# Kernel optimization log

Hardware: AMD Instinct MI355X
Metric: run time of the kernel (lower is better)

## Reference

```python
import jax, jax.numpy as jnp
import numpy as np

PAD = 7                 # init padding
T = 2 * PAD + 1         # T_side_dense = 15 shifts per axis
LAMDA = 1.0             # init lamda
EPS = 1e-16             # hardcoded epsilon in the torch loss body


def _joint_hist(x_out, x_tf_out):
    # Equivalent of F.conv2d(x_out.permute(1,0,2,3), weight=x_tf_out.permute(1,0,2,3), padding=PAD)
    # expressed as T*T shifted matmuls (correlation / cost-volume form).
    bn, k, h, w = x_out.shape
    A = jnp.transpose(x_out, (1, 0, 2, 3))      # (k, bn, h, w)  conv "input"
    B = jnp.transpose(x_tf_out, (1, 0, 2, 3))   # (k, bn, h, w)  conv "weight"
    A_pad = jnp.pad(A, ((0, 0), (0, 0), (PAD, PAD), (PAD, PAD)))

    def step(carry, s):
        dy, dx = s // T, s % T
        sl = jax.lax.dynamic_slice(A_pad, (0, 0, dy, dx), (k, bn, h, w))
        # p[n, o] at this shift = sum_{c,y,x} A_pad[n,c,y+dy,x+dx] * B[o,c,y,x]
        return carry, jnp.einsum('nchw,ochw->no', sl, B)

    _, p = jax.lax.scan(step, None, jnp.arange(T * T))
    # (T*T, k, k) -> (T, T, k, k); matches torch p_i_j.permute(2, 3, 0, 1)
    return p.reshape(T, T, k, k)


def reference(x_out, x_tf_out):
    p = _joint_hist(x_out, x_tf_out)
    # shift to positive; min is detached in torch -> stop_gradient
    p = p - jax.lax.stop_gradient(p.min()) + EPS
    # normalize per shift over the (k, k) joint
    p = p / p.sum(axis=(2, 3), keepdims=True)
    # symmetrize
    p = (p + jnp.swapaxes(p, 2, 3)) / 2.0
    p_i = p.sum(axis=2, keepdims=True)   # (T, T, 1, k) marginal (broadcasts like repeat)
    p_j = p.sum(axis=3, keepdims=True)   # (T, T, k, 1) marginal
    loss = (-p * (jnp.log(p + EPS)
                  - LAMDA * jnp.log(p_i + EPS)
                  - LAMDA * jnp.log(p_j + EPS))).sum() / (T * T)
    return loss


def setup_inputs() -> dict:
    key = jax.random.key(0)
    k1, k2 = jax.random.split(key)
    bn, k, h, w = 16, 10, 224, 224
    # simplex over axis=1 is asserted by the torch module -> use softmax
    x_out = jax.nn.softmax(jax.random.normal(k1, (bn, k, h, w), dtype=jnp.float32), axis=1)
    x_tf_out = jax.nn.softmax(jax.random.normal(k2, (bn, k, h, w), dtype=jnp.float32), axis=1)
    return {"x_out": x_out, "x_tf_out": x_tf_out}
```

## Files before the change

### kernel.cpp

```cpp
#include <hip/hip_runtime.h>
#include <stdint.h>
#include <math.h>


#define PADV 7
#define TS 15
#define KCLS 10
#define HH 224
#define WW 224
#define MD 160
#define NCELL (MD*MD)
#define NBLK 256
#define TY 14
#define BSTRIDE 232
#define BPH 240
#define PLANEE 2408
#define ABUFE (8*PLANEE)
#define LEPS 1e-16

typedef __attribute__((ext_vector_type(4))) float f32x4;
typedef __attribute__((ext_vector_type(8))) short bf16x8;

__device__ __forceinline__ unsigned short f2bf(float f) {
  union { float f; uint32_t u; } v; v.f = f;
  return (unsigned short)((v.u + 0x7FFFu + ((v.u >> 16) & 1u)) >> 16);
}

__device__ __forceinline__ uint32_t pack2bf(float a, float b) {
  return (uint32_t)f2bf(a) | ((uint32_t)f2bf(b) << 16);
}

__device__ __forceinline__ void glds16(const unsigned short* g, unsigned short* l) {
  __builtin_amdgcn_global_load_lds(
      (const __attribute__((address_space(1))) unsigned int*)g,
      (__attribute__((address_space(3))) unsigned int*)l, 16, 0, 0);
}

__device__ __forceinline__ void plane_write(const f32x4 f[4], unsigned short* awr) {
  uint32_t w[8];
#pragma unroll
  for (int k = 0; k < 8; ++k)
    w[k] = pack2bf(f[k >> 1][(k & 1) * 2], f[k >> 1][(k & 1) * 2 + 1]);
#pragma unroll
  for (int c = 0; c < 8; ++c) {
    union { uint32_t u[4]; uint4 v; } o;
    if (c & 1) {
#pragma unroll
      for (int j = 0; j < 4; ++j) o.u[j] = w[j + (c + 1) / 2];
    } else {
#pragma unroll
      for (int j = 0; j < 4; ++j)
        o.u[j] = __builtin_amdgcn_alignbit(w[j + 1 + c / 2], w[j + c / 2], 16);
    }
    *(uint4*)(awr + c * PLANEE) = o.v;
  }
}

__global__ __launch_bounds__(256)
void prep_b(const float* __restrict__ xt, unsigned short* __restrict__ bp) {
  const int idx   = blockIdx.x * 256 + threadIdx.x;
  const int rowid = idx / 29;
  const int chunk = idx - rowid * 29;
  const int x0    = chunk * 8;
  const int yy    = rowid % BPH;
  const int cls   = rowid / BPH;
  const int row   = yy - PADV;
  union { unsigned short h[8]; uint4 v; } out;
  if (row >= 0 && row < HH && x0 < WW) {
    const float* src = xt + ((size_t)cls * HH + row) * WW + x0;
#pragma unroll
    for (int j = 0; j < 8; ++j) out.h[j] = f2bf(src[j]);
  } else {
    out.v = make_uint4(0u, 0u, 0u, 0u);
  }
  *(uint4*)(bp + (size_t)rowid * BSTRIDE + x0) = out.v;
}

__global__ __launch_bounds__(640, 3)
void corr_gemm(const float* __restrict__ xo, const unsigned short* __restrict__ bpad,
               float* __restrict__ partials) {
  __shared__ __align__(16) unsigned short ldsA8[2 * ABUFE];
  __shared__ __align__(16) unsigned short ldsB[KCLS * 16 * BSTRIDE];

  const int tid  = threadIdx.x;
  const int bid0 = blockIdx.x;
  const int bid  = (bid0 & 7) * 32 + (bid0 >> 3);
  const int b    = bid >> 4;
  const int y0   = (bid & 15) * TY;

  const int lane = tid & 63;
  const int wv   = tid >> 6;
  const int wm   = wv >> 1;
  const int wn   = wv & 1;
  const int quad = lane >> 4;
  const int l15  = lane & 15;

  f32x4 acc[2][5];
#pragma unroll
  for (int i = 0; i < 2; ++i)
#pragma unroll
    for (int j = 0; j < 5; ++j) acc[i][j] = (f32x4){0.f, 0.f, 0.f, 0.f};

  const float* Ab = xo + (size_t)b * KCLS * HH * WW;
  const unsigned short* Bb = bpad + (size_t)b * KCLS * BPH * BSTRIDE;

  const bool aw  = tid < 300;
  const int an   = aw ? tid / 30 : 0;
  const int atp  = aw ? tid - (tid / 30) * 30 : 0;
  const int axb  = atp * 8 - 8;
  bool gv[4];
#pragma unroll
  for (int g = 0; g < 4; ++g)
    gv[g] = aw && (axb + 4 * g >= 0) && (axb + 4 * g + 4 <= WW);
  unsigned short* const awr0 = ldsA8 + an * 240 + atp * 8;

  for (int pr = wv; pr < 15 * KCLS; pr += 10) {
    const int r15  = pr / KCLS;
    const int o    = pr - r15 * KCLS;
    const int yy   = y0 + r15;
    const int slot = (y0 - PADV + r15) & 15;
    if (lane < 29)
      glds16(Bb + ((size_t)o * BPH + yy) * BSTRIDE + lane * 8,
             ldsB + (o * 16 + slot) * BSTRIDE);
  }

  f32x4 f[4];
  {
    const float* src = Ab + ((size_t)an * HH + y0) * WW + axb;
#pragma unroll
    for (int g = 0; g < 4; ++g) {
      f[g] = (f32x4){0.f, 0.f, 0.f, 0.f};
      if (gv[g]) f[g] = *(const f32x4*)(src + 4 * g);
    }
  }
  if (aw) plane_write(f, awr0);
  __syncthreads();

  int cur = 0;
  for (int s = 0; s < TY; ++s) {
    const int y = y0 + s;
    const bool more = (s + 1 < TY);

    if (more) {
      const int yy   = y + 8 + PADV;
      const int slot = (y + 8) & 15;
      if (lane < 29)
        glds16(Bb + ((size_t)wv * BPH + yy) * BSTRIDE + lane * 8,
               ldsB + (wv * 16 + slot) * BSTRIDE);
      const float* src = Ab + ((size_t)an * HH + (y + 1)) * WW + axb;
#pragma unroll
      for (int g = 0; g < 4; ++g) {
        f[g] = (f32x4){0.f, 0.f, 0.f, 0.f};
        if (gv[g]) f[g] = *(const f32x4*)(src + 4 * g);
      }
    }

    const unsigned short* paB = ldsA8 + cur * ABUFE + (l15 & 7) * PLANEE + (l15 & 8);
    const int slotB = (y + PADV - l15) & 15;

#pragma unroll 1
    for (int xc = 0; xc < 7; ++xc) {
      const int x0 = xc * 32;
      bf16x8 afrag[2], bfrag[5];
#pragma unroll
      for (int mi = 0; mi < 2; ++mi)
        afrag[mi] = *(const bf16x8*)(paB + (wm * 2 + mi) * 240 + x0 + quad * 8);
#pragma unroll
      for (int ni = 0; ni < 5; ++ni) {
        const int to = wn * 5 + ni;
        bfrag[ni] = *(const bf16x8*)(ldsB + (to * 16 + slotB) * BSTRIDE + x0 + quad * 8);
      }
#pragma unroll
      for (int mi = 0; mi < 2; ++mi)
#pragma unroll
        for (int ni = 0; ni < 5; ++ni)
          acc[mi][ni] = __builtin_amdgcn_mfma_f32_16x16x32_bf16(
              afrag[mi], bfrag[ni], acc[mi][ni], 0, 0, 0);
    }

    if (more) {
      if (aw) plane_write(f, awr0 + (cur ^ 1) * ABUFE);
      __syncthreads();
      cur ^= 1;
    }
  }

  float* outp = partials + (size_t)bid * NCELL;
#pragma unroll
  for (int mi = 0; mi < 2; ++mi)
#pragma unroll
    for (int ni = 0; ni < 5; ++ni) {
      const int mrow = (wm * 2 + mi) * 16 + quad * 4;
      const int ncol = (wn * 5 + ni) * 16 + l15;
#pragma unroll
      for (int r = 0; r < 4; ++r)
        outp[(size_t)(mrow + r) * MD + ncol] = acc[mi][ni][r];
    }
}

__global__ __launch_bounds__(256)
void reduce_stage1(const float* __restrict__ partials, float* __restrict__ stage2) {
  const int c  = (blockIdx.x % 100) * 256 + threadIdx.x;
  const int pg = blockIdx.x / 100;
  const float* base = partials + (size_t)pg * 32 * NCELL + c;
  float s0 = 0.f, s1 = 0.f, s2 = 0.f, s3 = 0.f;
  for (int p = 0; p < 32; p += 4) {
    s0 += base[(size_t)(p + 0) * NCELL];
    s1 += base[(size_t)(p + 1) * NCELL];
    s2 += base[(size_t)(p + 2) * NCELL];
    s3 += base[(size_t)(p + 3) * NCELL];
  }
  stage2[(size_t)pg * NCELL + c] = (s0 + s1) + (s2 + s3);
}

__global__ __launch_bounds__(256)
void reduce_final(const float* __restrict__ stage2, float* __restrict__ Cout,
                  float* __restrict__ mins, float* __restrict__ dout) {
  const int c = blockIdx.x * 256 + threadIdx.x;
  if (blockIdx.x == 0 && threadIdx.x == 0) dout[0] = 0.f;
  double s = 0.0;
#pragma unroll
  for (int pg = 0; pg < 8; ++pg) s += (double)stage2[(size_t)pg * NCELL + c];
  const float sf = (float)s;
  Cout[c] = sf;
  const int m  = c / MD;
  const int nn = c - m * MD;
  const bool valid = ((m & 15) < TS) && ((nn & 15) < TS);
  __shared__ float red[256];
  red[threadIdx.x] = valid ? sf : 3.4e38f;
  __syncthreads();
  for (int st = 128; st > 0; st >>= 1) {
    if (threadIdx.x < st)
      red[threadIdx.x] = fminf(red[threadIdx.x], red[threadIdx.x + st]);
    __syncthreads();
  }
  if (threadIdx.x == 0) mins[blockIdx.x] = red[0];
}

__global__ __launch_bounds__(128)
void loss_kernel(const float* __restrict__ Cmat, const float* __restrict__ mins,
                 float* __restrict__ dout) {
  const int s   = blockIdx.x;
  const int dy  = s / TS;
  const int dx  = s - dy * TS;
  const int tid = threadIdx.x;
  __shared__ float fm[128];
  __shared__ double q[100];
  __shared__ double sym[100];
  __shared__ double pi[10], pj[10];
  __shared__ double red[128];

  fm[tid] = (tid < 100) ? mins[tid] : 3.4e38f;
  __syncthreads();
  for (int st = 64; st > 0; st >>= 1) {
    if (tid < st) fm[tid] = fminf(fm[tid], fm[tid + st]);
    __syncthreads();
  }
  const double minv = (double)fm[0];
  __syncthreads();

  if (tid < 100) {
    const int n = tid / 10, o = tid - (tid / 10) * 10;
    const double v = (double)Cmat[(size_t)(n * 16 + dx) * MD + (o * 16 + dy)];
    q[tid] = v - minv + LEPS;
  }
  __syncthreads();
  red[tid] = (tid < 100) ? q[tid] : 0.0;
  __syncthreads();
  for (int st = 64; st > 0; st >>= 1) {
    if (tid < st) red[tid] += red[tid + st];
    __syncthreads();
  }
  const double Z = red[0];
  __syncthreads();
  if (tid < 100) {
    const int n = tid / 10, o = tid - (tid / 10) * 10;
    sym[tid] = (q[n * 10 + o] + q[o * 10 + n]) * 0.5 / Z;
  }
  __syncthreads();
  if (tid < 10) {
    double a = 0.0, bsum = 0.0;
    for (int n2 = 0; n2 < 10; ++n2) {
      a    += sym[n2 * 10 + tid];
      bsum += sym[tid * 10 + n2];
    }
    pi[tid] = a;
    pj[tid] = bsum;
  }
  __syncthreads();
  double term = 0.0;
  if (tid < 100) {
    const int n = tid / 10, o = tid - (tid / 10) * 10;
    const double sp = sym[tid];
    term = -sp * (log(sp + LEPS) - log(pi[o] + LEPS) - log(pj[n] + LEPS));
  }
  red[tid] = term;
  __syncthreads();
  for (int st = 64; st > 0; st >>= 1) {
    if (tid < st) red[tid] += red[tid + st];
    __syncthreads();
  }
  if (tid == 0) atomicAdd(dout, (float)(red[0] / (double)(TS * TS)));
}

extern "C" void kernel_launch(void* const* d_in, const int* in_sizes, int n_in,
                              void* d_out, int out_size, void* d_ws, size_t ws_size,
                              hipStream_t stream) {
  const float* xo = (const float*)d_in[0];
  const float* xt = (const float*)d_in[1];
  float* ws       = (float*)d_ws;

  float* partials = ws;
  float* stage2   = partials + (size_t)NBLK * NCELL;
  float* Cmat     = stage2 + (size_t)8 * NCELL;
  float* mins     = Cmat + NCELL;
  unsigned short* bpad = (unsigned short*)(mins + 128);
  float* out      = (float*)d_out;

  hipLaunchKernelGGL(prep_b,        dim3(4350), dim3(256), 0, stream, xt, bpad);
  hipLaunchKernelGGL(corr_gemm,     dim3(NBLK), dim3(640), 0, stream, xo, bpad, partials);
  hipLaunchKernelGGL(reduce_stage1, dim3(800),  dim3(256), 0, stream, partials, stage2);
  hipLaunchKernelGGL(reduce_final,  dim3(100),  dim3(256), 0, stream, stage2, Cmat, mins, out);
  hipLaunchKernelGGL(loss_kernel,   dim3(225),  dim3(128), 0, stream, Cmat, mins, out);
}
```

Measured before the change: 150.9 us.

## Split corr_gemm waves by K-range with LDS reduction and fuse reduce stages

The ten waves in each corr_gemm block are split into two K-groups that cover different x-chunk ranges. Each wave now computes a larger M×N tile, and four of the five waves in a group share their B fragments. The two groups' accumulators are summed through LDS before the block writes its partials, and only the second group issues the B-row prefetch. The two-stage partial reduction is merged into one kernel that reads all 256 partials in double precision, and prep_b loads with float4. In exchange, accumulator register use doubles, occupancy drops to 2 blocks per SM, and the fused reduction runs on only 100 blocks.

```diff
diff --git a/kernel.cpp b/kernel.cpp
--- a/kernel.cpp
+++ b/kernel.cpp
@@ -16,6 +16,8 @@
 #define BPH 240
 #define PLANEE 2408
 #define ABUFE (8*PLANEE)
+#define LDSA_BYTES (2*ABUFE*2)
+#define LDSB_BYTES (KCLS*16*BSTRIDE*2)
 #define LEPS 1e-16
 
 typedef __attribute__((ext_vector_type(4))) float f32x4;
@@ -53,6 +55,57 @@
         o.u[j] = __builtin_amdgcn_alignbit(w[j + 1 + c / 2], w[j + c / 2], 16);
     }
     *(uint4*)(awr + c * PLANEE) = o.v;
+  }
+}
+
+template<int XB, int XE>
+__device__ __forceinline__ void compute_xcs(
+    const unsigned short* __restrict__ paB, const unsigned short* __restrict__ lB,
+    int slotB, bool shareB, int Mb0, int Nb0, int q8, f32x4 (&acc)[2][2][5]) {
+#pragma unroll
+  for (int xc = XB; xc < XE; ++xc) {
+    const int qo = xc * 32 + q8;
+    if (shareB) {
+      bf16x8 bfrag[5];
+#pragma unroll
+      for (int ni = 0; ni < 5; ++ni)
+        bfrag[ni] = *(const bf16x8*)(lB + ((Nb0 + ni) * 16 + slotB) * BSTRIDE + qo);
+#pragma unroll
+      for (int sub = 0; sub < 2; ++sub) {
+        bf16x8 afrag[2];
+#pragma unroll
+        for (int mi = 0; mi < 2; ++mi)
+          afrag[mi] = *(const bf16x8*)(paB + (Mb0 + 2 * sub + mi) * 240 + qo);
+        __builtin_amdgcn_s_setprio(1);
+#pragma unroll
+        for (int mi = 0; mi < 2; ++mi)
+#pragma unroll
+          for (int ni = 0; ni < 5; ++ni)
+            acc[sub][mi][ni] = __builtin_amdgcn_mfma_f32_16x16x32_bf16(
+                afrag[mi], bfrag[ni], acc[sub][mi][ni], 0, 0, 0);
+        __builtin_amdgcn_s_setprio(0);
+      }
+    } else {
+      bf16x8 afrag[2];
+#pragma unroll
+      for (int mi = 0; mi < 2; ++mi)
+        afrag[mi] = *(const bf16x8*)(paB + (Mb0 + mi) * 240 + qo);
+#pragma unroll
+      for (int sub = 0; sub < 2; ++sub) {
+        bf16x8 bfrag[5];
+#pragma unroll
+        for (int ni = 0; ni < 5; ++ni)
+          bfrag[ni] = *(const bf16x8*)(lB + ((5 * sub + ni) * 16 + slotB) * BSTRIDE + qo);
+        __builtin_amdgcn_s_setprio(1);
+#pragma unroll
+        for (int mi = 0; mi < 2; ++mi)
+#pragma unroll
+          for (int ni = 0; ni < 5; ++ni)
+            acc[sub][mi][ni] = __builtin_amdgcn_mfma_f32_16x16x32_bf16(
+                afrag[mi], bfrag[ni], acc[sub][mi][ni], 0, 0, 0);
+        __builtin_amdgcn_s_setprio(0);
+      }
+    }
   }
 }
 
@@ -66,21 +119,26 @@
   const int cls   = rowid / BPH;
   const int row   = yy - PADV;
   union { unsigned short h[8]; uint4 v; } out;
-  if (row >= 0 && row < HH && x0 < WW) {
-    const float* src = xt + ((size_t)cls * HH + row) * WW + x0;
-#pragma unroll
-    for (int j = 0; j < 8; ++j) out.h[j] = f2bf(src[j]);
+  if (row >= 0 && row < HH && chunk < 28) {
+    const float4* src = (const float4*)(xt + ((size_t)cls * HH + row) * WW + x0);
+    const float4 f0 = src[0], f1 = src[1];
+    out.h[0] = f2bf(f0.x); out.h[1] = f2bf(f0.y);
+    out.h[2] = f2bf(f0.z); out.h[3] = f2bf(f0.w);
+    out.h[4] = f2bf(f1.x); out.h[5] = f2bf(f1.y);
+    out.h[6] = f2bf(f1.z); out.h[7] = f2bf(f1.w);
   } else {
     out.v = make_uint4(0u, 0u, 0u, 0u);
   }
   *(uint4*)(bp + (size_t)rowid * BSTRIDE + x0) = out.v;
 }
 
-__global__ __launch_bounds__(640, 3)
+__global__ __launch_bounds__(640, 2)
 void corr_gemm(const float* __restrict__ xo, const unsigned short* __restrict__ bpad,
                float* __restrict__ partials) {
-  __shared__ __align__(16) unsigned short ldsA8[2 * ABUFE];
-  __shared__ __align__(16) unsigned short ldsB[KCLS * 16 * BSTRIDE];
+  __shared__ __align__(16) unsigned char smem[LDSA_BYTES + LDSB_BYTES];
+  unsigned short* const ldsA8 = (unsigned short*)smem;
+  unsigned short* const ldsB  = (unsigned short*)(smem + LDSA_BYTES);
+  float* const scratch        = (float*)smem;
 
   const int tid  = threadIdx.x;
   const int bid0 = blockIdx.x;
@@ -90,16 +148,23 @@
 
   const int lane = tid & 63;
   const int wv   = tid >> 6;
-  const int wm   = wv >> 1;
-  const int wn   = wv & 1;
+  const int kg   = (wv >= 5);
+  const int w5   = kg ? wv - 5 : wv;
   const int quad = lane >> 4;
   const int l15  = lane & 15;
-
-  f32x4 acc[2][5];
-#pragma unroll
-  for (int i = 0; i < 2; ++i)
-#pragma unroll
-    for (int j = 0; j < 5; ++j) acc[i][j] = (f32x4){0.f, 0.f, 0.f, 0.f};
+  const int q8   = quad * 8;
+
+  const bool shareB = (w5 < 4);
+  const int Mb0 = shareB ? (w5 >> 1) * 4 : 8;
+  const int Nb0 = shareB ? (w5 & 1) * 5 : 0;
+
+  f32x4 acc[2][2][5];
+#pragma unroll
+  for (int s2 = 0; s2 < 2; ++s2)
+#pragma unroll
+    for (int i = 0; i < 2; ++i)
+#pragma unroll
+      for (int j = 0; j < 5; ++j) acc[s2][i][j] = (f32x4){0.f, 0.f, 0.f, 0.f};
 
   const float* Ab = xo + (size_t)b * KCLS * HH * WW;
   const unsigned short* Bb = bpad + (size_t)b * KCLS * BPH * BSTRIDE;
@@ -142,11 +207,17 @@
     const bool more = (s + 1 < TY);
 
     if (more) {
-      const int yy   = y + 8 + PADV;
-      const int slot = (y + 8) & 15;
-      if (lane < 29)
-        glds16(Bb + ((size_t)wv * BPH + yy) * BSTRIDE + lane * 8,
-               ldsB + (wv * 16 + slot) * BSTRIDE);
+      if (kg == 1) {
+        const int yy   = y + 8 + PADV;
+        const int slot = (y + 8) & 15;
+#pragma unroll
+        for (int j = 0; j < 2; ++j) {
+          const int ro = w5 * 2 + j;
+          if (lane < 29)
+            glds16(Bb + ((size_t)ro * BPH + yy) * BSTRIDE + lane * 8,
+                   ldsB + (ro * 16 + slot) * BSTRIDE);
+        }
+      }
       const float* src = Ab + ((size_t)an * HH + (y + 1)) * WW + axb;
 #pragma unroll
       for (int g = 0; g < 4; ++g) {
@@ -158,25 +229,10 @@
     const unsigned short* paB = ldsA8 + cur * ABUFE + (l15 & 7) * PLANEE + (l15 & 8);
     const int slotB = (y + PADV - l15) & 15;
 
-#pragma unroll 1
-    for (int xc = 0; xc < 7; ++xc) {
-      const int x0 = xc * 32;
-      bf16x8 afrag[2], bfrag[5];
-#pragma unroll
-      for (int mi = 0; mi < 2; ++mi)
-        afrag[mi] = *(const bf16x8*)(paB + (wm * 2 + mi) * 240 + x0 + quad * 8);
-#pragma unroll
-      for (int ni = 0; ni < 5; ++ni) {
-        const int to = wn * 5 + ni;
-        bfrag[ni] = *(const bf16x8*)(ldsB + (to * 16 + slotB) * BSTRIDE + x0 + quad * 8);
-      }
-#pragma unroll
-      for (int mi = 0; mi < 2; ++mi)
-#pragma unroll
-        for (int ni = 0; ni < 5; ++ni)
-          acc[mi][ni] = __builtin_amdgcn_mfma_f32_16x16x32_bf16(
-              afrag[mi], bfrag[ni], acc[mi][ni], 0, 0, 0);
-    }
+    if (kg == 0)
+      compute_xcs<0, 3>(paB, ldsB, slotB, shareB, Mb0, Nb0, q8, acc);
+    else
+      compute_xcs<3, 7>(paB, ldsB, slotB, shareB, Mb0, Nb0, q8, acc);
 
     if (more) {
       if (aw) plane_write(f, awr0 + (cur ^ 1) * ABUFE);
@@ -185,43 +241,57 @@
     }
   }
 
-  float* outp = partials + (size_t)bid * NCELL;
-#pragma unroll
-  for (int mi = 0; mi < 2; ++mi)
-#pragma unroll
-    for (int ni = 0; ni < 5; ++ni) {
-      const int mrow = (wm * 2 + mi) * 16 + quad * 4;
-      const int ncol = (wn * 5 + ni) * 16 + l15;
-#pragma unroll
-      for (int r = 0; r < 4; ++r)
-        outp[(size_t)(mrow + r) * MD + ncol] = acc[mi][ni][r];
-    }
+  __syncthreads();
+  if (kg == 1) {
+    float* dst = scratch + w5 * 5120 + lane * 4;
+#pragma unroll
+    for (int sub = 0; sub < 2; ++sub)
+#pragma unroll
+      for (int mi = 0; mi < 2; ++mi)
+#pragma unroll
+        for (int ni = 0; ni < 5; ++ni) {
+          const int t = (sub * 2 + mi) * 5 + ni;
+          *(f32x4*)(dst + t * 256) = acc[sub][mi][ni];
+        }
+  }
+  __syncthreads();
+  if (kg == 0) {
+    const float* src = scratch + w5 * 5120 + lane * 4;
+    float* outp = partials + (size_t)bid * NCELL;
+#pragma unroll
+    for (int sub = 0; sub < 2; ++sub)
+#pragma unroll
+      for (int mi = 0; mi < 2; ++mi)
+#pragma unroll
+        for (int ni = 0; ni < 5; ++ni) {
+          const int t = (sub * 2 + mi) * 5 + ni;
+          f32x4 o = *(const f32x4*)(src + t * 256);
+          o += acc[sub][mi][ni];
+          const int tm = shareB ? (Mb0 + 2 * sub + mi) : (8 + mi);
+          const int to = shareB ? (Nb0 + ni) : (5 * sub + ni);
+          const int mrow = tm * 16 + quad * 4;
+          const int ncol = to * 16 + l15;
+#pragma unroll
+          for (int r = 0; r < 4; ++r)
+            outp[(size_t)(mrow + r) * MD + ncol] = o[r];
+        }
+  }
 }
 
 __global__ __launch_bounds__(256)
-void reduce_stage1(const float* __restrict__ partials, float* __restrict__ stage2) {
-  const int c  = (blockIdx.x % 100) * 256 + threadIdx.x;
-  const int pg = blockIdx.x / 100;
-  const float* base = partials + (size_t)pg * 32 * NCELL + c;
-  float s0 = 0.f, s1 = 0.f, s2 = 0.f, s3 = 0.f;
-  for (int p = 0; p < 32; p += 4) {
-    s0 += base[(size_t)(p + 0) * NCELL];
-    s1 += base[(size_t)(p + 1) * NCELL];
-    s2 += base[(size_t)(p + 2) * NCELL];
-    s3 += base[(size_t)(p + 3) * NCELL];
-  }
-  stage2[(size_t)pg * NCELL + c] = (s0 + s1) + (s2 + s3);
-}
-
-__global__ __launch_bounds__(256)
-void reduce_final(const float* __restrict__ stage2, float* __restrict__ Cout,
-                  float* __restrict__ mins, float* __restrict__ dout) {
+void reduce_all(const float* __restrict__ partials, float* __restrict__ Cout,
+                float* __restrict__ mins, float* __restrict__ dout) {
   const int c = blockIdx.x * 256 + threadIdx.x;
   if (blockIdx.x == 0 && threadIdx.x == 0) dout[0] = 0.f;
-  double s = 0.0;
-#pragma unroll
-  for (int pg = 0; pg < 8; ++pg) s += (double)stage2[(size_t)pg * NCELL + c];
-  const float sf = (float)s;
+  const float* base = partials + c;
+  double s0 = 0.0, s1 = 0.0, s2 = 0.0, s3 = 0.0;
+  for (int p = 0; p < NBLK; p += 4) {
+    s0 += (double)base[(size_t)(p + 0) * NCELL];
+    s1 += (double)base[(size_t)(p + 1) * NCELL];
+    s2 += (double)base[(size_t)(p + 2) * NCELL];
+    s3 += (double)base[(size_t)(p + 3) * NCELL];
+  }
+  const float sf = (float)((s0 + s1) + (s2 + s3));
   Cout[c] = sf;
   const int m  = c / MD;
   const int nn = c - m * MD;
@@ -311,15 +381,13 @@
   float* ws       = (float*)d_ws;
 
   float* partials = ws;
-  float* stage2   = partials + (size_t)NBLK * NCELL;
-  float* Cmat     = stage2 + (size_t)8 * NCELL;
+  float* Cmat     = partials + (size_t)NBLK * NCELL;
   float* mins     = Cmat + NCELL;
   unsigned short* bpad = (unsigned short*)(mins + 128);
   float* out      = (float*)d_out;
 
-  hipLaunchKernelGGL(prep_b,        dim3(4350), dim3(256), 0, stream, xt, bpad);
-  hipLaunchKernelGGL(corr_gemm,     dim3(NBLK), dim3(640), 0, stream, xo, bpad, partials);
-  hipLaunchKernelGGL(reduce_stage1, dim3(800),  dim3(256), 0, stream, partials, stage2);
-  hipLaunchKernelGGL(reduce_final,  dim3(100),  dim3(256), 0, stream, stage2, Cmat, mins, out);
-  hipLaunchKernelGGL(loss_kernel,   dim3(225),  dim3(128), 0, stream, Cmat, mins, out);
-}
+  hipLaunchKernelGGL(prep_b,      dim3(4350), dim3(256), 0, stream, xt, bpad);
+  hipLaunchKernelGGL(corr_gemm,   dim3(NBLK), dim3(640), 0, stream, xo, bpad, partials);
+  hipLaunchKernelGGL(reduce_all,  dim3(100),  dim3(256), 0, stream, partials, Cmat, mins, out);
+  hipLaunchKernelGGL(loss_kernel, dim3(225),  dim3(128), 0, stream, Cmat, mins, out);
+}
```

Result: slower. 437.1 us (+189.6%).
